# Kernel optimization log

Measured on AMD Instinct MI355X. Metric: run time of the kernel, lower is better.

## Reference

```python
import jax, jax.numpy as jnp
import numpy as np

EMBED = 2048
HIDDEN = 2048
T = 32768


def setup_inputs() -> dict:
    key = jax.random.key(0)
    k1, k2, k3, k4 = jax.random.split(key, 4)
    s_x = 1.0 / np.sqrt(EMBED)
    s_h = 1.0 / np.sqrt(HIDDEN)
    return {
        "X_embeddings": jax.random.normal(k1, (T, EMBED), dtype=jnp.float32),
        "Wx": jax.random.normal(k2, (EMBED, HIDDEN), dtype=jnp.float32) * s_x,
        "Wh": jax.random.normal(k3, (HIDDEN, HIDDEN), dtype=jnp.float32) * s_h,
        "b": jax.random.normal(k4, (HIDDEN,), dtype=jnp.float32) * 0.01,
    }


def reference(X_embeddings, Wx, Wh, b):
    # FastRecurrentRunner: H[0] = 0; for t in 0..T-2: H[t+1] = cell(X[t], H[t])
    # cell(x, h) = tanh(x @ Wx + h @ Wh + b)  (Elman RNN cell)
    dtype = X_embeddings.dtype
    # Precompute input projections for all steps at once (one big GEMM).
    xproj = X_embeddings[:-1] @ Wx + b  # [T-1, HIDDEN]

    def step(h, xp):
        h_next = jnp.tanh(xp + h @ Wh)
        return h_next, h_next

    h0 = jnp.zeros((HIDDEN,), dtype=dtype)
    _, H_tail = jax.lax.scan(step, h0, xproj)  # [T-1, HIDDEN]
    H = jnp.concatenate([h0[None, :], H_tail], axis=0)  # [T, HIDDEN]
    return H
```

## Files before the change

kernel.cpp:

```cpp
#include <hip/hip_runtime.h>
#include <math.h>

#define T_STEPS 32768
#define HID 2048
#define EMB 2048

#define BM 64
#define BN 64
#define BK 16

__global__ __launch_bounds__(256) void xproj_gemm(const float* __restrict__ X,
                                                  const float* __restrict__ Wx,
                                                  const float* __restrict__ bias,
                                                  float* __restrict__ XPout)
{
    __shared__ __align__(16) float As[BK][BM];
    __shared__ __align__(16) float Bs[BK][BN];

    const int tid = threadIdx.x;
    const int m0 = blockIdx.y * BM;
    const int n0 = blockIdx.x * BN;

    const int tn = tid & 15;
    const int tm = tid >> 4;
    const int am = tid >> 2;
    const int ak = (tid & 3) << 2;
    const int bk = tid >> 4;
    const int bn = (tid & 15) << 2;

    const int arow = m0 + am;
    const bool aval = arow < (T_STEPS - 1);

    float acc[4][4];
#pragma unroll
    for (int i = 0; i < 4; ++i)
#pragma unroll
        for (int j = 0; j < 4; ++j) acc[i][j] = 0.f;

    for (int k0 = 0; k0 < EMB; k0 += BK) {
        float4 av = make_float4(0.f, 0.f, 0.f, 0.f);
        if (aval) av = *(const float4*)&X[(size_t)arow * EMB + k0 + ak];
        float4 bv = *(const float4*)&Wx[(size_t)(k0 + bk) * HID + n0 + bn];

        __syncthreads();
        As[ak + 0][am] = av.x;
        As[ak + 1][am] = av.y;
        As[ak + 2][am] = av.z;
        As[ak + 3][am] = av.w;
        *(float4*)&Bs[bk][bn] = bv;
        __syncthreads();

#pragma unroll
        for (int k = 0; k < BK; ++k) {
            float4 a4 = *(const float4*)&As[k][tm << 2];
            float4 b4 = *(const float4*)&Bs[k][tn << 2];
            acc[0][0] += a4.x * b4.x; acc[0][1] += a4.x * b4.y;
            acc[0][2] += a4.x * b4.z; acc[0][3] += a4.x * b4.w;
            acc[1][0] += a4.y * b4.x; acc[1][1] += a4.y * b4.y;
            acc[1][2] += a4.y * b4.z; acc[1][3] += a4.y * b4.w;
            acc[2][0] += a4.z * b4.x; acc[2][1] += a4.z * b4.y;
            acc[2][2] += a4.z * b4.z; acc[2][3] += a4.z * b4.w;
            acc[3][0] += a4.w * b4.x; acc[3][1] += a4.w * b4.y;
            acc[3][2] += a4.w * b4.z; acc[3][3] += a4.w * b4.w;
        }
    }

    float4 bb = *(const float4*)&bias[n0 + (tn << 2)];
#pragma unroll
    for (int i = 0; i < 4; ++i) {
        int m = m0 + (tm << 2) + i;
        if (m < T_STEPS - 1) {
            float4 o;
            o.x = acc[i][0] + bb.x;
            o.y = acc[i][1] + bb.y;
            o.z = acc[i][2] + bb.z;
            o.w = acc[i][3] + bb.w;
            *(float4*)&XPout[(size_t)m * HID + n0 + (tn << 2)] = o;
        }
    }
}

typedef int v4i __attribute__((ext_vector_type(4)));
typedef int v2i __attribute__((ext_vector_type(2)));

__device__ __forceinline__ float dot4(float4 a, float4 b)
{
    return a.x * b.x + a.y * b.y + a.z * b.z + a.w * b.w;
}

__device__ __forceinline__ void poll2_sc0(const void* p, v4i& a, v4i& b)
{
    asm volatile("global_load_dwordx4 %0, %2, off sc0\n\t"
                 "global_load_dwordx4 %1, %2, off offset:16 sc0\n\t"
                 "s_waitcnt vmcnt(0)"
                 : "=&v"(a), "=&v"(b) : "v"(p) : "memory");
}
__device__ __forceinline__ void poll2_sys(const void* p, v4i& a, v4i& b)
{
    asm volatile("global_load_dwordx4 %0, %2, off sc0 sc1\n\t"
                 "global_load_dwordx4 %1, %2, off offset:16 sc0 sc1\n\t"
                 "s_waitcnt vmcnt(0)"
                 : "=&v"(a), "=&v"(b) : "v"(p) : "memory");
}
__device__ __forceinline__ void st8_sc0(void* p, v2i v)
{
    asm volatile("global_store_dwordx2 %0, %1, off sc0" :: "v"(p), "v"(v) : "memory");
}
__device__ __forceinline__ void st8_sys(void* p, v2i v)
{
    asm volatile("global_store_dwordx2 %0, %1, off sc0 sc1" :: "v"(p), "v"(v) : "memory");
}

__device__ __forceinline__ unsigned short bf16rne(float f)
{
    unsigned u = __float_as_uint(f);
    u += 0x7fffu + ((u >> 16) & 1u);
    return (unsigned short)(u >> 16);
}
__device__ __forceinline__ float bfup(unsigned short s)
{
    return __uint_as_float((unsigned)s << 16);
}

#define SCAN_TPB 512

__global__ __launch_bounds__(SCAN_TPB, 1) void rnn_scan_fast(const float* __restrict__ Wh,
                                                             const float* __restrict__ XP,
                                                             float* __restrict__ H,
                                                             unsigned long long* __restrict__ hcomm)
{
    __shared__ __align__(16) ushort4 Wb[8][20][64];
    __shared__ __align__(16) float hlds[2][HID];
    __shared__ float pacc[8][64];

    const int tid = threadIdx.x;
    const int wave = tid >> 6;
    const int lane = tid & 63;
    const int g = blockIdx.x & 7;
    const int rank = blockIdx.x >> 3;
    const int bc0 = rank * 64;
    unsigned long long* hcg = hcomm + (size_t)g * (2 * HID);

    float4 wreg[44];
    {
        const float* wp = Wh + (size_t)(256 * wave) * HID + bc0 + lane;
#pragma unroll
        for (int i = 0; i < 44; ++i) {
            wreg[i].x = wp[(size_t)(4 * i + 0) * HID];
            wreg[i].y = wp[(size_t)(4 * i + 1) * HID];
            wreg[i].z = wp[(size_t)(4 * i + 2) * HID];
            wreg[i].w = wp[(size_t)(4 * i + 3) * HID];
        }
    }
    for (int j = 0; j < 20; ++j) {
        const float* p = Wh + (size_t)(256 * wave + 176 + 4 * j) * HID + bc0 + lane;
        ushort4 u;
        u.x = bf16rne(p[0]);
        u.y = bf16rne(p[(size_t)HID]);
        u.z = bf16rne(p[2 * (size_t)HID]);
        u.w = bf16rne(p[3 * (size_t)HID]);
        Wb[wave][j][lane] = u;
    }
    __syncthreads();

    for (int t = 0; t < T_STEPS - 1; ++t) {
        const int par = t & 1;

        float xpv = 0.f;
        if (wave == 0) xpv = XP[(size_t)t * HID + bc0 + lane];

        const char* pb = (const char*)hcg + (((size_t)par * HID + 4 * (size_t)tid) << 3);
        v4i e0, e1;
        int round = 0;
        for (;;) {
            if ((round & 15) == 15) poll2_sys(pb, e0, e1);
            else                    poll2_sc0(pb, e0, e1);
            if (((e0.y ^ t) | (e0.w ^ t) | (e1.y ^ t) | (e1.w ^ t)) == 0) break;
            ++round;
        }

        v4i hv; hv.x = e0.x; hv.y = e0.z; hv.z = e1.x; hv.w = e1.z;
        *(v4i*)&hlds[par][4 * tid] = hv;
        __syncthreads();

        const float* hb = &hlds[par][256 * wave];
        float a0 = 0.f, a1 = 0.f;
#pragma unroll
        for (int i = 0; i < 44; i += 2) {
            a0 += dot4(wreg[i],     *(const float4*)&hb[4 * i]);
            a1 += dot4(wreg[i + 1], *(const float4*)&hb[4 * i + 4]);
        }
        float b0 = 0.f;
#pragma unroll
        for (int j = 0; j < 20; ++j) {
            ushort4 u = Wb[wave][j][lane];
            float4 q = *(const float4*)&hb[176 + 4 * j];
            b0 += bfup(u.x) * q.x + bfup(u.y) * q.y
                + bfup(u.z) * q.z + bfup(u.w) * q.w;
        }
        pacc[wave][lane] = (a0 + a1) + b0;
        __syncthreads();

        if (wave == 0) {
            float tot = ((pacc[0][lane] + pacc[1][lane]) + (pacc[2][lane] + pacc[3][lane]))
                      + ((pacc[4][lane] + pacc[5][lane]) + (pacc[6][lane] + pacc[7][lane]));
            float hvn = tanhf(xpv + tot);
            v2i e; e.x = __float_as_int(hvn); e.y = t + 1;
            char* pa = (char*)hcg + (((size_t)(par ^ 1) * HID + bc0 + lane) << 3);
            st8_sys(pa, e);
            st8_sc0(pa, e);
            if (g == 0) H[(size_t)(t + 1) * HID + bc0 + lane] = hvn;
        }
    }
}

#define NBLK_R3 64
#define TPB_R3 1024
#define CPB_R3 32
#define CPW_R3 2

__device__ __forceinline__ v4i uncached_load16(const void* p)
{
    v4i r;
    asm volatile("global_load_dwordx4 %0, %1, off sc0 sc1\n\t"
                 "s_waitcnt vmcnt(0)"
                 : "=v"(r) : "v"(p) : "memory");
    return r;
}
__device__ __forceinline__ void uncached_store16(void* p, v4i v)
{
    asm volatile("global_store_dwordx4 %0, %1, off sc0 sc1"
                 :: "v"(p), "v"(v) : "memory");
}

__global__ __launch_bounds__(TPB_R3, 4) void rnn_scan_r3(const float* __restrict__ Wh,
                                                         float* __restrict__ H,
                                                         unsigned long long* __restrict__ hcomm)
{
    __shared__ __align__(16) float hlds[2][HID];
    __shared__ float pad[18432];

    const int tid = threadIdx.x;
    const int wave = tid >> 6;
    const int lane = tid & 63;
    const int c0 = blockIdx.x * CPB_R3 + wave * CPW_R3;

    if ((((size_t)hcomm) >> 22) & 1) ((volatile float*)pad)[tid] = 0.f;

    float4 w0[8], w1[8];
#pragma unroll
    for (int k = 0; k < 8; ++k) {
        const int r = 4 * lane + 256 * k;
        const float* p = Wh + (size_t)r * HID + c0;
        w0[k].x = p[0];                     w1[k].x = p[1];
        w0[k].y = p[(size_t)HID];           w1[k].y = p[(size_t)HID + 1];
        w0[k].z = p[(size_t)(2 * HID)];     w1[k].z = p[(size_t)(2 * HID) + 1];
        w0[k].w = p[(size_t)(3 * HID)];     w1[k].w = p[(size_t)(3 * HID) + 1];
    }

    for (int t = 0; t < T_STEPS - 1; ++t) {
        float2 xp = make_float2(0.f, 0.f);
        if (lane == 0) xp = *(const float2*)&H[(size_t)(t + 1) * HID + c0];

        const char* slot = (const char*)hcomm +
                           (((size_t)(t & 1) * HID + 2 * (size_t)tid) << 3);
        v4i e;
        do {
            e = uncached_load16(slot);
        } while (e.y != t || e.w != t);

        *(float2*)&hlds[t & 1][2 * tid] =
            make_float2(__int_as_float(e.x), __int_as_float(e.z));
        __syncthreads();

        const float* hb = hlds[t & 1];
        float s0 = 0.f, s1 = 0.f;
#pragma unroll
        for (int k = 0; k < 8; ++k) {
            float4 hh = *(const float4*)&hb[4 * lane + 256 * k];
            s0 += hh.x * w0[k].x + hh.y * w0[k].y + hh.z * w0[k].z + hh.w * w0[k].w;
            s1 += hh.x * w1[k].x + hh.y * w1[k].y + hh.z * w1[k].z + hh.w * w1[k].w;
        }
#pragma unroll
        for (int m = 1; m < 64; m <<= 1) {
            s0 += __shfl_xor(s0, m, 64);
            s1 += __shfl_xor(s1, m, 64);
        }

        if (lane == 0) {
            float h0 = tanhf(xp.x + s0);
            float h1 = tanhf(xp.y + s1);
            v4i pub;
            pub.x = __float_as_int(h0); pub.y = t + 1;
            pub.z = __float_as_int(h1); pub.w = t + 1;
            uncached_store16((char*)hcomm +
                             (((size_t)((t + 1) & 1) * HID + (size_t)c0) << 3), pub);
            *(float2*)&H[(size_t)(t + 1) * HID + c0] = make_float2(h0, h1);
        }
    }
}

static void launch_r3_path(const float* X, const float* Wx, const float* Wh,
                           const float* b, float* H, void* d_ws, hipStream_t stream)
{
    unsigned long long* hcomm = (unsigned long long*)d_ws;
    hipMemsetAsync(H, 0, HID * sizeof(float), stream);
    hipMemsetAsync(d_ws, 0, 2 * HID * sizeof(unsigned long long), stream);

    dim3 ggrid(HID / BN, T_STEPS / BM);
    xproj_gemm<<<ggrid, 256, 0, stream>>>(X, Wx, b, H + HID);

    const float* whp = Wh; float* hp = H; unsigned long long* cp = hcomm;
    void* args[] = { (void*)&whp, (void*)&hp, (void*)&cp };
    hipLaunchCooperativeKernel((const void*)rnn_scan_r3, dim3(NBLK_R3),
                               dim3(TPB_R3), args, 0, stream);
}

extern "C" void kernel_launch(void* const* d_in, const int* in_sizes, int n_in,
                              void* d_out, int out_size, void* d_ws, size_t ws_size,
                              hipStream_t stream)
{
    const float* X  = (const float*)d_in[0];
    const float* Wx = (const float*)d_in[1];
    const float* Wh = (const float*)d_in[2];
    const float* b  = (const float*)d_in[3];
    float* H = (float*)d_out;

    const size_t XP_BYTES = (size_t)(T_STEPS - 1) * HID * sizeof(float);
    const size_t XP_OFF   = 512 * 1024;
    const bool big_ws = ws_size >= XP_OFF + XP_BYTES;

    int nb = 0;
    bool fast_ok = big_ws &&
        (hipOccupancyMaxActiveBlocksPerMultiprocessor(&nb, (const void*)rnn_scan_fast,
                                                      SCAN_TPB, 0) == hipSuccess) && nb >= 1;

    if (fast_ok) {
        unsigned long long* hcomm = (unsigned long long*)d_ws;
        float* XPb = (float*)((char*)d_ws + XP_OFF);

        hipMemsetAsync(H, 0, HID * sizeof(float), stream);
        hipMemsetAsync(d_ws, 0, 8 * 2 * HID * sizeof(unsigned long long), stream);

        dim3 ggrid(HID / BN, T_STEPS / BM);
        xproj_gemm<<<ggrid, 256, 0, stream>>>(X, Wx, b, XPb);

        const float* whp = Wh; const float* xpp = XPb;
        float* hp = H; unsigned long long* cp = hcomm;
        void* args[] = { (void*)&whp, (void*)&xpp, (void*)&hp, (void*)&cp };
        hipError_t err = hipLaunchCooperativeKernel((const void*)rnn_scan_fast,
                                                    dim3(256), dim3(SCAN_TPB), args, 0, stream);
        if (err != hipSuccess) {
            launch_r3_path(X, Wx, Wh, b, H, d_ws, stream);
        }
    } else {
        launch_r3_path(X, Wx, Wh, b, H, d_ws, stream);
    }
}
```

Baseline: 138.6 ms.

## Split recurrent scan across twice as many smaller blocks with wider polling

The persistent scan kernel now launches 512 blocks of 256 threads instead of 256 blocks of 512. Each block owns 32 hidden columns, and each wave's two half-waves cover separate 256-row K slices. Each thread now polls 64 bytes of the shared hidden-state exchange buffer per step, and switches to system-scope loads after the third round on alternate rounds. The intent is to spread per-step work and the cross-block reduction over two co-resident blocks per CU with shorter intra-block barriers. The cost is double the global polling traffic per step, and the launcher now needs two blocks per CU, otherwise it falls back to the slower path.

Result: no change. 141.2 ms (+1.9%).

```diff
diff --git a/kernel.cpp b/kernel.cpp
--- a/kernel.cpp
+++ b/kernel.cpp
@@ -88,19 +88,23 @@
     return a.x * b.x + a.y * b.y + a.z * b.z + a.w * b.w;
 }
 
-__device__ __forceinline__ void poll2_sc0(const void* p, v4i& a, v4i& b)
-{
-    asm volatile("global_load_dwordx4 %0, %2, off sc0\n\t"
-                 "global_load_dwordx4 %1, %2, off offset:16 sc0\n\t"
+__device__ __forceinline__ void poll4_sc0(const void* p, v4i& a, v4i& b, v4i& c, v4i& d)
+{
+    asm volatile("global_load_dwordx4 %0, %4, off sc0\n\t"
+                 "global_load_dwordx4 %1, %4, off offset:16 sc0\n\t"
+                 "global_load_dwordx4 %2, %4, off offset:32 sc0\n\t"
+                 "global_load_dwordx4 %3, %4, off offset:48 sc0\n\t"
                  "s_waitcnt vmcnt(0)"
-                 : "=&v"(a), "=&v"(b) : "v"(p) : "memory");
-}
-__device__ __forceinline__ void poll2_sys(const void* p, v4i& a, v4i& b)
-{
-    asm volatile("global_load_dwordx4 %0, %2, off sc0 sc1\n\t"
-                 "global_load_dwordx4 %1, %2, off offset:16 sc0 sc1\n\t"
+                 : "=&v"(a), "=&v"(b), "=&v"(c), "=&v"(d) : "v"(p) : "memory");
+}
+__device__ __forceinline__ void poll4_sys(const void* p, v4i& a, v4i& b, v4i& c, v4i& d)
+{
+    asm volatile("global_load_dwordx4 %0, %4, off sc0 sc1\n\t"
+                 "global_load_dwordx4 %1, %4, off offset:16 sc0 sc1\n\t"
+                 "global_load_dwordx4 %2, %4, off offset:32 sc0 sc1\n\t"
+                 "global_load_dwordx4 %3, %4, off offset:48 sc0 sc1\n\t"
                  "s_waitcnt vmcnt(0)"
-                 : "=&v"(a), "=&v"(b) : "v"(p) : "memory");
+                 : "=&v"(a), "=&v"(b), "=&v"(c), "=&v"(d) : "v"(p) : "memory");
 }
 __device__ __forceinline__ void st8_sc0(void* p, v2i v)
 {
@@ -122,28 +126,33 @@
     return __uint_as_float((unsigned)s << 16);
 }
 
-#define SCAN_TPB 512
+#define SCAN_TPB 256
+#define NBLK_FAST 512
 
 __global__ __launch_bounds__(SCAN_TPB, 1) void rnn_scan_fast(const float* __restrict__ Wh,
                                                              const float* __restrict__ XP,
                                                              float* __restrict__ H,
                                                              unsigned long long* __restrict__ hcomm)
 {
-    __shared__ __align__(16) ushort4 Wb[8][20][64];
+    __shared__ __align__(16) ushort4 Wb[4][2][20][32];
     __shared__ __align__(16) float hlds[2][HID];
-    __shared__ float pacc[8][64];
+    __shared__ float pacc[4][2][32];
 
     const int tid = threadIdx.x;
     const int wave = tid >> 6;
     const int lane = tid & 63;
+    const int half = lane >> 5;
+    const int lcol = lane & 31;
     const int g = blockIdx.x & 7;
     const int rank = blockIdx.x >> 3;
-    const int bc0 = rank * 64;
+    const int bc0 = rank * 32;
+    const int col = bc0 + lcol;
+    const int rb = 512 * wave + 256 * half;
     unsigned long long* hcg = hcomm + (size_t)g * (2 * HID);
 
     float4 wreg[44];
     {
-        const float* wp = Wh + (size_t)(256 * wave) * HID + bc0 + lane;
+        const float* wp = Wh + (size_t)rb * HID + col;
 #pragma unroll
         for (int i = 0; i < 44; ++i) {
             wreg[i].x = wp[(size_t)(4 * i + 0) * HID];
@@ -153,13 +162,13 @@
         }
     }
     for (int j = 0; j < 20; ++j) {
-        const float* p = Wh + (size_t)(256 * wave + 176 + 4 * j) * HID + bc0 + lane;
+        const float* p = Wh + (size_t)(rb + 176 + 4 * j) * HID + col;
         ushort4 u;
         u.x = bf16rne(p[0]);
         u.y = bf16rne(p[(size_t)HID]);
         u.z = bf16rne(p[2 * (size_t)HID]);
         u.w = bf16rne(p[3 * (size_t)HID]);
-        Wb[wave][j][lane] = u;
+        Wb[wave][half][j][lcol] = u;
     }
     __syncthreads();
 
@@ -167,23 +176,26 @@
         const int par = t & 1;
 
         float xpv = 0.f;
-        if (wave == 0) xpv = XP[(size_t)t * HID + bc0 + lane];
-
-        const char* pb = (const char*)hcg + (((size_t)par * HID + 4 * (size_t)tid) << 3);
-        v4i e0, e1;
+        if (wave == 0 && lane < 32) xpv = XP[(size_t)t * HID + bc0 + lane];
+
+        const char* pb = (const char*)hcg + (((size_t)par * HID + 8 * (size_t)tid) << 3);
+        v4i e0, e1, e2, e3;
         int round = 0;
         for (;;) {
-            if ((round & 15) == 15) poll2_sys(pb, e0, e1);
-            else                    poll2_sc0(pb, e0, e1);
-            if (((e0.y ^ t) | (e0.w ^ t) | (e1.y ^ t) | (e1.w ^ t)) == 0) break;
+            if (round >= 3 && (round & 1)) poll4_sys(pb, e0, e1, e2, e3);
+            else                           poll4_sc0(pb, e0, e1, e2, e3);
+            if (((e0.y ^ t) | (e0.w ^ t) | (e1.y ^ t) | (e1.w ^ t) |
+                 (e2.y ^ t) | (e2.w ^ t) | (e3.y ^ t) | (e3.w ^ t)) == 0) break;
             ++round;
         }
 
-        v4i hv; hv.x = e0.x; hv.y = e0.z; hv.z = e1.x; hv.w = e1.z;
-        *(v4i*)&hlds[par][4 * tid] = hv;
-        __syncthreads();
-
-        const float* hb = &hlds[par][256 * wave];
+        v4i h0; h0.x = e0.x; h0.y = e0.z; h0.z = e1.x; h0.w = e1.z;
+        v4i h1; h1.x = e2.x; h1.y = e2.z; h1.z = e3.x; h1.w = e3.z;
+        *(v4i*)&hlds[par][8 * tid] = h0;
+        *(v4i*)&hlds[par][8 * tid + 4] = h1;
+        __syncthreads();
+
+        const float* hb = &hlds[par][rb];
         float a0 = 0.f, a1 = 0.f;
 #pragma unroll
         for (int i = 0; i < 44; i += 2) {
@@ -193,17 +205,19 @@
         float b0 = 0.f;
 #pragma unroll
         for (int j = 0; j < 20; ++j) {
-            ushort4 u = Wb[wave][j][lane];
+            ushort4 u = Wb[wave][half][j][lcol];
             float4 q = *(const float4*)&hb[176 + 4 * j];
             b0 += bfup(u.x) * q.x + bfup(u.y) * q.y
                 + bfup(u.z) * q.z + bfup(u.w) * q.w;
         }
-        pacc[wave][lane] = (a0 + a1) + b0;
-        __syncthreads();
-
-        if (wave == 0) {
-            float tot = ((pacc[0][lane] + pacc[1][lane]) + (pacc[2][lane] + pacc[3][lane]))
-                      + ((pacc[4][lane] + pacc[5][lane]) + (pacc[6][lane] + pacc[7][lane]));
+        pacc[wave][half][lcol] = (a0 + a1) + b0;
+        __syncthreads();
+
+        if (wave == 0 && lane < 32) {
+            float tot = ((pacc[0][0][lane] + pacc[0][1][lane])
+                       + (pacc[1][0][lane] + pacc[1][1][lane]))
+                      + ((pacc[2][0][lane] + pacc[2][1][lane])
+                       + (pacc[3][0][lane] + pacc[3][1][lane]));
             float hvn = tanhf(xpv + tot);
             v2i e; e.x = __float_as_int(hvn); e.y = t + 1;
             char* pa = (char*)hcg + (((size_t)(par ^ 1) * HID + bc0 + lane) << 3);
@@ -333,7 +347,7 @@
     int nb = 0;
     bool fast_ok = big_ws &&
         (hipOccupancyMaxActiveBlocksPerMultiprocessor(&nb, (const void*)rnn_scan_fast,
-                                                      SCAN_TPB, 0) == hipSuccess) && nb >= 1;
+                                                      SCAN_TPB, 0) == hipSuccess) && nb >= 2;
 
     if (fast_ok) {
         unsigned long long* hcomm = (unsigned long long*)d_ws;
@@ -349,7 +363,8 @@
         float* hp = H; unsigned long long* cp = hcomm;
         void* args[] = { (void*)&whp, (void*)&xpp, (void*)&hp, (void*)&cp };
         hipError_t err = hipLaunchCooperativeKernel((const void*)rnn_scan_fast,
-                                                    dim3(256), dim3(SCAN_TPB), args, 0, stream);
+                                                    dim3(NBLK_FAST), dim3(SCAN_TPB),
+                                                    args, 0, stream);
         if (err != hipSuccess) {
             launch_r3_path(X, Wx, Wh, b, H, d_ws, stream);
         }
```
